# Kernel tuning notes

Measured on AMD Instinct MI355X. Metric: run time of the kernel, lower is better.

The kernel has to match this reference:

```python
import jax, jax.numpy as jnp
import numpy as np

N = 100000   # total nodes in batch
E = 400000   # total directed edges
G = 4096     # number of graphs
D = 300      # emb_dim
H = 600      # GIN MLP hidden = 2*emb_dim
L = 5        # num_layer
BN_EPS = 1e-5
SELF_LOOP_BOND_TYPE = 4  # contextpred convention


def setup_inputs() -> dict:
    key = jax.random.key(0)
    ks = jax.random.split(key, 16)
    s = 0.1
    return {
        "x": jax.random.randint(ks[0], (N, 2), 0, 3),
        "edge_index": jax.random.randint(ks[1], (2, E), 0, N),
        "edge_attr": jax.random.randint(ks[2], (E, 2), 0, 3),
        "batch": jnp.sort(jax.random.randint(ks[3], (N,), 0, G)),
        "atom_emb1": jax.random.normal(ks[4], (120, D), jnp.float32) * s,
        "atom_emb2": jax.random.normal(ks[5], (3, D), jnp.float32) * s,
        "edge_emb1": jax.random.normal(ks[6], (L, 6, D), jnp.float32) * s,
        "edge_emb2": jax.random.normal(ks[7], (L, 3, D), jnp.float32) * s,
        "w1": jax.random.normal(ks[8], (L, D, H), jnp.float32) * (1.0 / np.sqrt(D)),
        "b1": jnp.zeros((L, H), jnp.float32),
        "w2": jax.random.normal(ks[9], (L, H, D), jnp.float32) * (1.0 / np.sqrt(H)),
        "b2": jnp.zeros((L, D), jnp.float32),
        "bn_g": jnp.ones((L, D), jnp.float32),
        "bn_b": jnp.zeros((L, D), jnp.float32),
        "bn_m": jnp.zeros((L, D), jnp.float32),
        "bn_v": jnp.ones((L, D), jnp.float32),
        "head_w1": jax.random.normal(ks[10], (D, 512), jnp.float32) * (1.0 / np.sqrt(D)),
        "head_b1": jnp.zeros((512,), jnp.float32),
        "head_w2": jax.random.normal(ks[11], (512, 2), jnp.float32) * (1.0 / np.sqrt(512)),
        "head_b2": jnp.zeros((2,), jnp.float32),
    }


def _gnn_forward(x, edge_index, edge_attr, batch,
                 atom_emb1, atom_emb2, edge_emb1, edge_emb2,
                 w1, b1, w2, b2, bn_g, bn_b, bn_m, bn_v,
                 head_w1, head_b1, head_w2, head_b2):
    src, dst = edge_index[0], edge_index[1]
    # node input embedding: atom type + chirality
    h = atom_emb1[x[:, 0]] + atom_emb2[x[:, 1]]  # [N, D]
    for l in range(L):
        # edge embeddings for real edges
        eemb = edge_emb1[l][edge_attr[:, 0]] + edge_emb2[l][edge_attr[:, 1]]  # [E, D]
        # self-loop edge embedding (bond type 4, direction 0), same for all nodes
        self_emb = edge_emb1[l][SELF_LOOP_BOND_TYPE] + edge_emb2[l][0]  # [D]
        # GIN 'add' aggregation of messages (x_j + edge_emb), incl. self loops
        agg = jax.ops.segment_sum(h[src] + eemb, dst, num_segments=N)
        agg = agg + h + self_emb  # fused self-loop contribution
        # MLP: Linear(D,2D) -> ReLU -> Linear(2D,D)
        h = jax.nn.relu(agg @ w1[l] + b1[l]) @ w2[l] + b2[l]
        # BatchNorm1d in eval mode (running stats)
        h = (h - bn_m[l]) * jax.lax.rsqrt(bn_v[l] + BN_EPS) * bn_g[l] + bn_b[l]
        if l < L - 1:  # JK='last': ReLU on all but last layer
            h = jax.nn.relu(h)
    # to_dense_batch + sum(axis=1) == segment sum over graphs
    pooled = jax.ops.segment_sum(h, batch, num_segments=G)  # [G, D]
    # task head
    logits = jax.nn.relu(pooled @ head_w1 + head_b1) @ head_w2 + head_b2  # [G, 2]
    return logits


def reference(x, edge_index, edge_attr, batch,
              atom_emb1, atom_emb2, edge_emb1, edge_emb2,
              w1, b1, w2, b2, bn_g, bn_b, bn_m, bn_v,
              head_w1, head_b1, head_w2, head_b2):
    return _gnn_forward(x, edge_index, edge_attr, batch,
                        atom_emb1, atom_emb2, edge_emb1, edge_emb2,
                        w1, b1, w2, b2, bn_g, bn_b, bn_m, bn_v,
                        head_w1, head_b1, head_w2, head_b2)
```

## Files before the change

kernel.cpp:

```cpp
#include <hip/hip_runtime.h>
#include <hip/hip_bf16.h>
#include <stdint.h>

#define N_NODES 100000
#define N_EDGES 400000
#define N_GRAPH 4096
#define DIMD    300
#define NLAYER  5
#define HPAD   304
#define KP1    320
#define W1ROWS 640
#define WID2   320
#define MROWS  64
#define HGR    64

typedef __attribute__((ext_vector_type(8))) short bf16x8_t;
typedef __attribute__((ext_vector_type(4))) float f32x4_t;

__device__ __forceinline__ void gload_lds16(const void* g, void* l) {
  auto gp = (__attribute__((address_space(1))) void*)(uintptr_t)g;
  auto lp = (__attribute__((address_space(3))) void*)(uint32_t)(uintptr_t)l;
  __builtin_amdgcn_global_load_lds(gp, lp, 16, 0, 0);
}
__device__ __forceinline__ short f2bs(float f) {
  __hip_bfloat16 b = __float2bfloat16(f); return *(short*)&b;
}
__device__ __forceinline__ float bs2f(short s) {
  __hip_bfloat16 b; *(short*)&b = s; return __bfloat162float(b);
}
__device__ __forceinline__ void soft_barrier() {
  asm volatile("s_waitcnt lgkmcnt(0)" ::: "memory");
  __builtin_amdgcn_s_barrier();
}

__global__ void k_hist(const int* __restrict__ ei, int* __restrict__ cur) {
  const int e = blockIdx.x * blockDim.x + threadIdx.x;
  if (e < N_EDGES) atomicAdd(&cur[ei[N_EDGES + e]], 1);
}

__global__ void k_scan1(int* __restrict__ cur, int* __restrict__ off, int* __restrict__ bsum) {
  __shared__ int buf[1024];
  const int tid = threadIdx.x;
  const int i = blockIdx.x * 1024 + tid;
  int v = (i < N_NODES) ? cur[i] : 0;
  buf[tid] = v;
  __syncthreads();
  for (int s = 1; s < 1024; s <<= 1) {
    int t = (tid >= s) ? buf[tid - s] : 0;
    __syncthreads();
    buf[tid] += t;
    __syncthreads();
  }
  if (i < N_NODES) { off[i + 1] = buf[tid]; cur[i] = 0; }
  if (tid == 1023) bsum[blockIdx.x] = buf[1023];
}

__global__ void k_scan2(int* __restrict__ bsum, int nb) {
  if (threadIdx.x == 0 && blockIdx.x == 0) {
    int run = 0;
    for (int b = 0; b < nb; ++b) { int v = bsum[b]; bsum[b] = run; run += v; }
  }
}

__global__ void k_scan3(int* __restrict__ off, const int* __restrict__ bsum) {
  const int i = blockIdx.x * blockDim.x + threadIdx.x;
  if (i == 0) off[0] = 0;
  if (i < N_NODES) off[i + 1] += bsum[i >> 10];
}

__global__ void k_fill(const int* __restrict__ ei, const int* __restrict__ ea,
                       const int* __restrict__ off, int* __restrict__ cur,
                       int* __restrict__ csr) {
  const int e = blockIdx.x * blockDim.x + threadIdx.x;
  if (e < N_EDGES) {
    const int d = ei[N_EDGES + e];
    const int pos = atomicAdd(&cur[d], 1);
    const int c = ea[2 * e] * 3 + ea[2 * e + 1];
    csr[off[d] + pos] = (ei[e] << 4) | c;
  }
}

__global__ void k_comb(const float* __restrict__ e1, const float* __restrict__ e2,
                       float* __restrict__ comb) {
  const int idx = blockIdx.x * blockDim.x + threadIdx.x;
  if (idx >= NLAYER * 10 * HPAD) return;
  const int l = idx / (10 * HPAD);
  const int r = (idx / HPAD) % 10;
  const int d = idx % HPAD;
  float v = 0.f;
  if (d < DIMD) {
    int a, b;
    if (r < 9) { a = r / 3; b = r % 3; } else { a = 4; b = 0; }
    v = e1[(l * 6 + a) * DIMD + d] + e2[(l * 3 + b) * DIMD + d];
  }
  comb[idx] = v;
}

__global__ void k_wc1(const float* __restrict__ w, __hip_bfloat16* __restrict__ wb) {
  const int idx = blockIdx.x * blockDim.x + threadIdx.x;
  if (idx >= NLAYER * W1ROWS * KP1) return;
  const int l = idx / (W1ROWS * KP1);
  const int n = (idx / KP1) % W1ROWS;
  const int k = idx % KP1;
  float v = 0.f;
  if (n < 600 && k < DIMD) v = w[((long)l * DIMD + k) * 600 + n];
  wb[idx] = __float2bfloat16(v);
}

__global__ void k_wc2(const float* __restrict__ w, __hip_bfloat16* __restrict__ wb) {
  const int idx = blockIdx.x * blockDim.x + threadIdx.x;
  if (idx >= NLAYER * WID2 * W1ROWS) return;
  const int l = idx / (WID2 * W1ROWS);
  const int n = (idx / W1ROWS) % WID2;
  const int k = idx % W1ROWS;
  float v = 0.f;
  if (n < DIMD && k < 600) v = w[((long)l * 600 + k) * DIMD + n];
  wb[idx] = __float2bfloat16(v);
}

__global__ void k_wch(const float* __restrict__ w, __hip_bfloat16* __restrict__ wb) {
  const int idx = blockIdx.x * blockDim.x + threadIdx.x;
  if (idx >= 512 * KP1) return;
  const int n = idx / KP1;
  const int k = idx % KP1;
  float v = (k < DIMD) ? w[(long)k * 512 + n] : 0.f;
  wb[idx] = __float2bfloat16(v);
}

__global__ void k_nemb(const int* __restrict__ x, const float* __restrict__ ae1,
                       const float* __restrict__ ae2, __hip_bfloat16* __restrict__ h) {
  const int gid = blockIdx.x * blockDim.x + threadIdx.x;
  if (gid >= N_NODES * 38) return;
  const int node = gid / 38;
  const int l = gid % 38;
  bf16x8_t ov;
#pragma unroll
  for (int j = 0; j < 8; ++j) ov[j] = 0;
  {
    const int i0 = x[2 * node], i1 = x[2 * node + 1];
    const float* r1 = ae1 + (long)i0 * DIMD + l * 8;
    const float* r2 = ae2 + (long)i1 * DIMD + l * 8;
#pragma unroll
    for (int j = 0; j < 8; ++j) {
      const int d = l * 8 + j;
      if (d < DIMD) ov[j] = f2bs(r1[j] + r2[j]);
    }
  }
  *(bf16x8_t*)(h + (long)node * HPAD + l * 8) = ov;
}

__global__ __launch_bounds__(256)
void k_agg(const __hip_bfloat16* __restrict__ h, __hip_bfloat16* __restrict__ aggb,
           const int* __restrict__ csr, const int* __restrict__ off,
           const float* __restrict__ comb) {
  const int wv = threadIdx.x >> 6;
  const int lane = threadIdx.x & 63;
  const int node = blockIdx.x * 4 + wv;
  if (node >= N_NODES) return;
  if (lane >= 40) return;
  const bool act = lane < 38;
  float acc[8];
  if (act) {
    const bf16x8_t hv = *(const bf16x8_t*)(h + (long)node * HPAD + lane * 8);
    const float* c9 = comb + 9 * HPAD + lane * 8;
#pragma unroll
    for (int j = 0; j < 8; ++j) acc[j] = bs2f(hv[j]) + c9[j];
  } else {
#pragma unroll
    for (int j = 0; j < 8; ++j) acc[j] = 0.f;
  }
  const int p0 = off[node], p1 = off[node + 1];
  int p = p0;
  for (; p + 1 < p1; p += 2) {
    const int v0 = csr[p], v1 = csr[p + 1];
    if (act) {
      const bf16x8_t h0 = *(const bf16x8_t*)(h + (long)(v0 >> 4) * HPAD + lane * 8);
      const bf16x8_t h1 = *(const bf16x8_t*)(h + (long)(v1 >> 4) * HPAD + lane * 8);
      const float* c0 = comb + (v0 & 15) * HPAD + lane * 8;
      const float* c1 = comb + (v1 & 15) * HPAD + lane * 8;
#pragma unroll
      for (int j = 0; j < 8; ++j) acc[j] += bs2f(h0[j]) + c0[j];
#pragma unroll
      for (int j = 0; j < 8; ++j) acc[j] += bs2f(h1[j]) + c1[j];
    }
  }
  if (p < p1) {
    const int v0 = csr[p];
    if (act) {
      const bf16x8_t h0 = *(const bf16x8_t*)(h + (long)(v0 >> 4) * HPAD + lane * 8);
      const float* c0 = comb + (v0 & 15) * HPAD + lane * 8;
#pragma unroll
      for (int j = 0; j < 8; ++j) acc[j] += bs2f(h0[j]) + c0[j];
    }
  }
  bf16x8_t ov;
#pragma unroll
  for (int j = 0; j < 8; ++j) ov[j] = act ? f2bs(acc[j]) : (short)0;
  *(bf16x8_t*)(aggb + (long)node * KP1 + lane * 8) = ov;
}

__global__ __launch_bounds__(256)
void k_mlp(const __hip_bfloat16* __restrict__ aggb,
           const __hip_bfloat16* __restrict__ w1b,
           const __hip_bfloat16* __restrict__ w2b,
           const float* __restrict__ b1,
           const float* __restrict__ b2,
           const float* __restrict__ bng, const float* __restrict__ bnb,
           const float* __restrict__ bnm, const float* __restrict__ bnv,
           int reluFlag,
           __hip_bfloat16* __restrict__ h) {
  __shared__ __align__(16) char As[MROWS * 640];
  __shared__ __align__(16) char P[2 * MROWS * 256];
  const int tid = threadIdx.x;
  const int lane = tid & 63;
  const int wc = tid >> 6;
  const int fr = lane & 15;
  const int kg = lane >> 4;
  const int row0 = blockIdx.x * MROWS;

#pragma unroll
  for (int it = 0; it < 10; ++it) {
    const int g = it * 256 + tid;
    const int r = g / 40;
    const int gin = g - r * 40;
    int ar = row0 + r;
    if (ar >= N_NODES) ar = N_NODES - 1;
    gload_lds16((const char*)aggb + (size_t)ar * 640 + (size_t)((gin ^ (r & 7)) * 16),
                As + g * 16);
  }

  f32x4_t accB[4][5];
#pragma unroll
  for (int m = 0; m < 4; ++m)
#pragma unroll
    for (int n = 0; n < 5; ++n) accB[m][n] = (f32x4_t){0.f, 0.f, 0.f, 0.f};

  __syncthreads();

  {
    f32x4_t accA[4][2];
#pragma unroll
    for (int m = 0; m < 4; ++m)
#pragma unroll
      for (int n = 0; n < 2; ++n) accA[m][n] = (f32x4_t){0.f, 0.f, 0.f, 0.f};
    const __hip_bfloat16* w1c = w1b + (size_t)(wc * 32) * KP1;
#pragma unroll
    for (int ks = 0; ks < 10; ++ks) {
      const int k2 = ks * 64 + kg * 16;
      bf16x8_t af[4], bfr[2];
#pragma unroll
      for (int m = 0; m < 4; ++m) {
        const int r = m * 16 + fr;
        af[m] = *(const bf16x8_t*)(As + r * 640 + (k2 ^ ((r & 7) << 4)));
      }
#pragma unroll
      for (int n = 0; n < 2; ++n)
        bfr[n] = *(const bf16x8_t*)(w1c + (size_t)(n * 16 + fr) * KP1 + ks * 32 + kg * 8);
#pragma unroll
      for (int m = 0; m < 4; ++m)
#pragma unroll
        for (int n = 0; n < 2; ++n)
          accA[m][n] = __builtin_amdgcn_mfma_f32_16x16x32_bf16(af[m], bfr[n], accA[m][n], 0, 0, 0);
    }
#pragma unroll
    for (int n = 0; n < 2; ++n) {
      const int col = wc * 32 + n * 16 + fr;
      const float bv = (col < 600) ? b1[col] : 0.f;
#pragma unroll
      for (int m = 0; m < 4; ++m)
#pragma unroll
        for (int j = 0; j < 4; ++j) {
          const int prow = m * 16 + kg * 4 + j;
          const int pcol = wc * 32 + n * 16 + fr;
          *(short*)(P + prow * 256 + ((pcol * 2) ^ ((prow & 7) << 4))) =
              f2bs(fmaxf(accA[m][n][j] + bv, 0.f));
        }
    }
  }
  soft_barrier();

#pragma unroll
  for (int c = 0; c < 5; ++c) {
    const char* Pc = P + (c & 1) * (MROWS * 256);
    char* Pn = P + ((c + 1) & 1) * (MROWS * 256);

    bf16x8_t w1f[10];
    if (c < 4) {
      const __hip_bfloat16* w1c = w1b + (size_t)((c + 1) * 128 + wc * 32) * KP1;
#pragma unroll
      for (int ks = 0; ks < 5; ++ks)
#pragma unroll
        for (int n = 0; n < 2; ++n)
          w1f[ks * 2 + n] = *(const bf16x8_t*)(w1c + (size_t)(n * 16 + fr) * KP1 + ks * 32 + kg * 8);
    }

#pragma unroll
    for (int ks = 0; ks < 4; ++ks) {
      bf16x8_t af2[4], bf2[5];
#pragma unroll
      for (int m = 0; m < 4; ++m) {
        const int pr = m * 16 + fr;
        af2[m] = *(const bf16x8_t*)(Pc + pr * 256 + ((ks * 64 + kg * 16) ^ ((pr & 7) << 4)));
      }
      const int k2 = c * 128 + ks * 32 + kg * 8;
#pragma unroll
      for (int n = 0; n < 5; ++n)
        bf2[n] = *(const bf16x8_t*)(w2b + (size_t)(wc * 80 + n * 16 + fr) * W1ROWS + k2);
#pragma unroll
      for (int m = 0; m < 4; ++m)
#pragma unroll
        for (int n = 0; n < 5; ++n)
          accB[m][n] = __builtin_amdgcn_mfma_f32_16x16x32_bf16(af2[m], bf2[n], accB[m][n], 0, 0, 0);
    }

    if (c < 4) {
      f32x4_t accA[4][2];
#pragma unroll
      for (int m = 0; m < 4; ++m)
#pragma unroll
        for (int n = 0; n < 2; ++n) accA[m][n] = (f32x4_t){0.f, 0.f, 0.f, 0.f};
      const __hip_bfloat16* w1c = w1b + (size_t)((c + 1) * 128 + wc * 32) * KP1;
#pragma unroll
      for (int ks = 0; ks < 5; ++ks) {
        const int k2 = ks * 64 + kg * 16;
        bf16x8_t af[4];
#pragma unroll
        for (int m = 0; m < 4; ++m) {
          const int r = m * 16 + fr;
          af[m] = *(const bf16x8_t*)(As + r * 640 + (k2 ^ ((r & 7) << 4)));
        }
#pragma unroll
        for (int m = 0; m < 4; ++m)
#pragma unroll
          for (int n = 0; n < 2; ++n)
            accA[m][n] = __builtin_amdgcn_mfma_f32_16x16x32_bf16(af[m], w1f[ks * 2 + n], accA[m][n], 0, 0, 0);
      }
#pragma unroll
      for (int ks = 5; ks < 10; ++ks) {
        const int k2 = ks * 64 + kg * 16;
        bf16x8_t af[4], bfr[2];
#pragma unroll
        for (int m = 0; m < 4; ++m) {
          const int r = m * 16 + fr;
          af[m] = *(const bf16x8_t*)(As + r * 640 + (k2 ^ ((r & 7) << 4)));
        }
#pragma unroll
        for (int n = 0; n < 2; ++n)
          bfr[n] = *(const bf16x8_t*)(w1c + (size_t)(n * 16 + fr) * KP1 + ks * 32 + kg * 8);
#pragma unroll
        for (int m = 0; m < 4; ++m)
#pragma unroll
          for (int n = 0; n < 2; ++n)
            accA[m][n] = __builtin_amdgcn_mfma_f32_16x16x32_bf16(af[m], bfr[n], accA[m][n], 0, 0, 0);
      }
#pragma unroll
      for (int n = 0; n < 2; ++n) {
        const int col = (c + 1) * 128 + wc * 32 + n * 16 + fr;
        const float bv = (col < 600) ? b1[col] : 0.f;
#pragma unroll
        for (int m = 0; m < 4; ++m)
#pragma unroll
          for (int j = 0; j < 4; ++j) {
            const int prow = m * 16 + kg * 4 + j;
            const int pcol = wc * 32 + n * 16 + fr;
            *(short*)(Pn + prow * 256 + ((pcol * 2) ^ ((prow & 7) << 4))) =
                f2bs(fmaxf(accA[m][n][j] + bv, 0.f));
          }
      }
    }
    soft_barrier();
  }

  float scale[5], shift[5];
#pragma unroll
  for (int n = 0; n < 5; ++n) {
    const int col = wc * 80 + n * 16 + fr;
    if (col < DIMD) {
      const float sc = rsqrtf(bnv[col] + 1e-5f) * bng[col];
      scale[n] = sc;
      shift[n] = (b2[col] - bnm[col]) * sc + bnb[col];
    } else { scale[n] = 0.f; shift[n] = 0.f; }
  }
#pragma unroll
  for (int m = 0; m < 4; ++m) {
#pragma unroll
    for (int n = 0; n < 5; ++n) {
      const int col = wc * 80 + n * 16 + fr;
      if (col >= HPAD) continue;
#pragma unroll
      for (int j = 0; j < 4; ++j) {
        const int node = row0 + m * 16 + kg * 4 + j;
        if (node >= N_NODES) continue;
        float v = 0.f;
        if (col < DIMD) {
          v = accB[m][n][j] * scale[n] + shift[n];
          if (reluFlag) v = fmaxf(v, 0.f);
        }
        h[(size_t)node * HPAD + col] = __float2bfloat16(v);
      }
    }
  }
}

__device__ __forceinline__ int lbound(const int* a, int n, int key) {
  int lo = 0, hi = n;
  while (lo < hi) { int mid = (lo + hi) >> 1; if (a[mid] < key) lo = mid + 1; else hi = mid; }
  return lo;
}

__global__ void k_pool(const __hip_bfloat16* __restrict__ h, const int* __restrict__ batch,
                       __hip_bfloat16* __restrict__ pooled) {
  __shared__ int se[2];
  const int g = blockIdx.x;
  if (threadIdx.x < 2) se[threadIdx.x] = lbound(batch, N_NODES, g + threadIdx.x);
  __syncthreads();
  const int d = threadIdx.x;
  if (d < KP1) {
    float a = 0.f;
    if (d < DIMD)
      for (int i = se[0]; i < se[1]; ++i) a += __bfloat162float(h[(long)i * HPAD + d]);
    pooled[(long)g * KP1 + d] = __float2bfloat16(d < DIMD ? a : 0.f);
  }
}

__global__ __launch_bounds__(256)
void k_head(const __hip_bfloat16* __restrict__ pooled,
            const __hip_bfloat16* __restrict__ hw1b,
            const float* __restrict__ hb1, const float* __restrict__ hw2,
            const float* __restrict__ hb2, float* __restrict__ out) {
  __shared__ __align__(16) char As[HGR * 640];
  __shared__ float sred[4][HGR][2];
  const int tid = threadIdx.x;
  const int lane = tid & 63;
  const int wc = tid >> 6;
  const int fr = lane & 15;
  const int kg = lane >> 4;
  const int g0 = blockIdx.x * HGR;

#pragma unroll
  for (int it = 0; it < 10; ++it) {
    const int g = it * 256 + tid;
    const int r = g / 40;
    const int gin = g - r * 40;
    gload_lds16((const char*)pooled + (size_t)(g0 + r) * 640 + (size_t)((gin ^ (r & 7)) * 16),
                As + g * 16);
  }

  f32x4_t acc[4][8];
#pragma unroll
  for (int m = 0; m < 4; ++m)
#pragma unroll
    for (int n = 0; n < 8; ++n) acc[m][n] = (f32x4_t){0.f, 0.f, 0.f, 0.f};

  __syncthreads();

#pragma unroll
  for (int ks = 0; ks < 10; ++ks) {
    const int k2 = ks * 64 + kg * 16;
    bf16x8_t af[4], bw[8];
#pragma unroll
    for (int m = 0; m < 4; ++m) {
      const int r = m * 16 + fr;
      af[m] = *(const bf16x8_t*)(As + r * 640 + (k2 ^ ((r & 7) << 4)));
    }
#pragma unroll
    for (int n = 0; n < 8; ++n)
      bw[n] = *(const bf16x8_t*)(hw1b + (size_t)(wc * 128 + n * 16 + fr) * KP1 + ks * 32 + kg * 8);
#pragma unroll
    for (int m = 0; m < 4; ++m)
#pragma unroll
      for (int n = 0; n < 8; ++n)
        acc[m][n] = __builtin_amdgcn_mfma_f32_16x16x32_bf16(af[m], bw[n], acc[m][n], 0, 0, 0);
  }

  float p0[4][4], p1[4][4];
#pragma unroll
  for (int m = 0; m < 4; ++m)
#pragma unroll
    for (int j = 0; j < 4; ++j) { p0[m][j] = 0.f; p1[m][j] = 0.f; }
#pragma unroll
  for (int n = 0; n < 8; ++n) {
    const int col = wc * 128 + n * 16 + fr;
    const float bv = hb1[col];
    const float wa = hw2[2 * col], wb = hw2[2 * col + 1];
#pragma unroll
    for (int m = 0; m < 4; ++m)
#pragma unroll
      for (int j = 0; j < 4; ++j) {
        const float z = fmaxf(acc[m][n][j] + bv, 0.f);
        p0[m][j] = fmaf(z, wa, p0[m][j]);
        p1[m][j] = fmaf(z, wb, p1[m][j]);
      }
  }
#pragma unroll
  for (int m = 0; m < 4; ++m)
#pragma unroll
    for (int j = 0; j < 4; ++j) {
#pragma unroll
      for (int s = 1; s < 16; s <<= 1) {
        p0[m][j] += __shfl_xor(p0[m][j], s, 64);
        p1[m][j] += __shfl_xor(p1[m][j], s, 64);
      }
    }
  if (fr == 0) {
#pragma unroll
    for (int m = 0; m < 4; ++m)
#pragma unroll
      for (int j = 0; j < 4; ++j) {
        const int row = m * 16 + kg * 4 + j;
        sred[wc][row][0] = p0[m][j];
        sred[wc][row][1] = p1[m][j];
      }
  }
  __syncthreads();
  if (tid < HGR) {
    const int row = tid;
    float a0 = sred[0][row][0] + sred[1][row][0] + sred[2][row][0] + sred[3][row][0];
    float a1 = sred[0][row][1] + sred[1][row][1] + sred[2][row][1] + sred[3][row][1];
    out[2 * (g0 + row)] = a0 + hb2[0];
    out[2 * (g0 + row) + 1] = a1 + hb2[1];
  }
}

__global__ void k_sentinel(float* out) { out[threadIdx.x] = 1.0e6f; }

extern "C" void kernel_launch(void* const* d_in, const int* in_sizes, int n_in,
                              void* d_out, int out_size, void* d_ws, size_t ws_size,
                              hipStream_t stream) {
  const int*   x     = (const int*)d_in[0];
  const int*   ei    = (const int*)d_in[1];
  const int*   ea    = (const int*)d_in[2];
  const int*   batch = (const int*)d_in[3];
  const float* ae1   = (const float*)d_in[4];
  const float* ae2   = (const float*)d_in[5];
  const float* ee1   = (const float*)d_in[6];
  const float* ee2   = (const float*)d_in[7];
  const float* w1    = (const float*)d_in[8];
  const float* b1    = (const float*)d_in[9];
  const float* w2    = (const float*)d_in[10];
  const float* b2    = (const float*)d_in[11];
  const float* bng   = (const float*)d_in[12];
  const float* bnbp  = (const float*)d_in[13];
  const float* bnm   = (const float*)d_in[14];
  const float* bnv   = (const float*)d_in[15];
  const float* hw1   = (const float*)d_in[16];
  const float* hb1   = (const float*)d_in[17];
  const float* hw2   = (const float*)d_in[18];
  const float* hb2   = (const float*)d_in[19];
  float* out = (float*)d_out;

  char* ws = (char*)d_ws;
  size_t o = 0;
  auto alloc = [&](size_t bytes) { size_t p = o; o += (bytes + 255) & ~(size_t)255; return p; };
  __hip_bfloat16* h      = (__hip_bfloat16*)(ws + alloc((size_t)N_NODES * HPAD * 2));
  __hip_bfloat16* aggb   = (__hip_bfloat16*)(ws + alloc((size_t)N_NODES * KP1 * 2));
  __hip_bfloat16* w1b    = (__hip_bfloat16*)(ws + alloc((size_t)NLAYER * W1ROWS * KP1 * 2));
  __hip_bfloat16* w2b    = (__hip_bfloat16*)(ws + alloc((size_t)NLAYER * WID2 * W1ROWS * 2));
  __hip_bfloat16* hw1b   = (__hip_bfloat16*)(ws + alloc((size_t)512 * KP1 * 2));
  float*          comb   = (float*)         (ws + alloc((size_t)NLAYER * 10 * HPAD * 4));
  int*            offp   = (int*)           (ws + alloc((size_t)(N_NODES + 1) * 4));
  int*            cur    = (int*)           (ws + alloc((size_t)N_NODES * 4));
  int*            csr    = (int*)           (ws + alloc((size_t)N_EDGES * 4));
  __hip_bfloat16* pooled = (__hip_bfloat16*)(ws + alloc((size_t)N_GRAPH * KP1 * 2));
  int*            bsum   = (int*)           (ws + alloc(128 * 4));
  if (o > ws_size) {
    k_sentinel<<<1, 8, 0, stream>>>(out);
    return;
  }

  hipMemsetAsync(cur, 0, (size_t)N_NODES * 4, stream);

  k_hist<<<(N_EDGES + 255) / 256, 256, 0, stream>>>(ei, cur);
  const int nsb = (N_NODES + 1023) / 1024;
  k_scan1<<<nsb, 1024, 0, stream>>>(cur, offp, bsum);
  k_scan2<<<1, 64, 0, stream>>>(bsum, nsb);
  k_scan3<<<(N_NODES + 255) / 256, 256, 0, stream>>>(offp, bsum);
  k_fill<<<(N_EDGES + 255) / 256, 256, 0, stream>>>(ei, ea, offp, cur, csr);

  k_wc1<<<(NLAYER * W1ROWS * KP1 + 255) / 256, 256, 0, stream>>>(w1, w1b);
  k_wc2<<<(NLAYER * WID2 * W1ROWS + 255) / 256, 256, 0, stream>>>(w2, w2b);
  k_wch<<<(512 * KP1 + 255) / 256, 256, 0, stream>>>(hw1, hw1b);
  k_comb<<<(NLAYER * 10 * HPAD + 255) / 256, 256, 0, stream>>>(ee1, ee2, comb);
  k_nemb<<<(N_NODES * 38 + 255) / 256, 256, 0, stream>>>(x, ae1, ae2, h);

  const int mlpBlocks = (N_NODES + MROWS - 1) / MROWS;
  for (int l = 0; l < NLAYER; ++l) {
    k_agg<<<(N_NODES + 3) / 4, 256, 0, stream>>>(h, aggb, csr, offp, comb + l * 10 * HPAD);
    k_mlp<<<mlpBlocks, 256, 0, stream>>>(aggb,
        w1b + (size_t)l * W1ROWS * KP1, w2b + (size_t)l * WID2 * W1ROWS,
        b1 + l * 600, b2 + l * DIMD,
        bng + l * DIMD, bnbp + l * DIMD, bnm + l * DIMD, bnv + l * DIMD,
        (l < NLAYER - 1) ? 1 : 0, h);
  }

  k_pool<<<N_GRAPH, KP1, 0, stream>>>(h, batch, pooled);
  k_head<<<N_GRAPH / HGR, 256, 0, stream>>>(pooled, hw1b, hb1, hw2, hb2, out);
}
```

Baseline: 1.782 ms.

## Replace double-buffered 128-col MLP chunks with simple 64-col loop and two barriers

Restructures the fused MLP kernel's hidden-dimension loop. The old version used double-buffered 128-column chunks of the hidden activation, with W1 fragments prefetched into registers and split GEMM1 stages. The new version uses a plain rolled loop over ten 64-column chunks, a single-buffered P tile that is half the size, and two full __syncthreads per chunk. This cuts LDS use and register pressure (fewer accumulators and no prefetch array), which may raise occupancy. In exchange it gives up the overlap between the two GEMMs and adds more barriers.

```diff
diff --git a/kernel.cpp b/kernel.cpp
--- a/kernel.cpp
+++ b/kernel.cpp
@@ -27,10 +27,6 @@
 }
 __device__ __forceinline__ float bs2f(short s) {
   __hip_bfloat16 b; *(short*)&b = s; return __bfloat162float(b);
-}
-__device__ __forceinline__ void soft_barrier() {
-  asm volatile("s_waitcnt lgkmcnt(0)" ::: "memory");
-  __builtin_amdgcn_s_barrier();
 }
 
 __global__ void k_hist(const int* __restrict__ ei, int* __restrict__ cur) {
@@ -210,7 +206,7 @@
            int reluFlag,
            __hip_bfloat16* __restrict__ h) {
   __shared__ __align__(16) char As[MROWS * 640];
-  __shared__ __align__(16) char P[2 * MROWS * 256];
+  __shared__ __align__(16) char P[MROWS * 128];
   const int tid = threadIdx.x;
   const int lane = tid & 63;
   const int wc = tid >> 6;
@@ -237,72 +233,49 @@
 
   __syncthreads();
 
-  {
-    f32x4_t accA[4][2];
-#pragma unroll
-    for (int m = 0; m < 4; ++m)
-#pragma unroll
-      for (int n = 0; n < 2; ++n) accA[m][n] = (f32x4_t){0.f, 0.f, 0.f, 0.f};
-    const __hip_bfloat16* w1c = w1b + (size_t)(wc * 32) * KP1;
+  for (int hc = 0; hc < 10; ++hc) {
+    f32x4_t accA[4];
+#pragma unroll
+    for (int m = 0; m < 4; ++m) accA[m] = (f32x4_t){0.f, 0.f, 0.f, 0.f};
+    const __hip_bfloat16* w1c = w1b + (size_t)(hc * 64 + wc * 16) * KP1;
 #pragma unroll
     for (int ks = 0; ks < 10; ++ks) {
       const int k2 = ks * 64 + kg * 16;
-      bf16x8_t af[4], bfr[2];
+      bf16x8_t af[4];
 #pragma unroll
       for (int m = 0; m < 4; ++m) {
         const int r = m * 16 + fr;
         af[m] = *(const bf16x8_t*)(As + r * 640 + (k2 ^ ((r & 7) << 4)));
       }
-#pragma unroll
-      for (int n = 0; n < 2; ++n)
-        bfr[n] = *(const bf16x8_t*)(w1c + (size_t)(n * 16 + fr) * KP1 + ks * 32 + kg * 8);
+      const bf16x8_t bfr = *(const bf16x8_t*)(w1c + (size_t)fr * KP1 + ks * 32 + kg * 8);
 #pragma unroll
       for (int m = 0; m < 4; ++m)
-#pragma unroll
-        for (int n = 0; n < 2; ++n)
-          accA[m][n] = __builtin_amdgcn_mfma_f32_16x16x32_bf16(af[m], bfr[n], accA[m][n], 0, 0, 0);
-    }
-#pragma unroll
-    for (int n = 0; n < 2; ++n) {
-      const int col = wc * 32 + n * 16 + fr;
-      const float bv = (col < 600) ? b1[col] : 0.f;
-#pragma unroll
-      for (int m = 0; m < 4; ++m)
-#pragma unroll
-        for (int j = 0; j < 4; ++j) {
-          const int prow = m * 16 + kg * 4 + j;
-          const int pcol = wc * 32 + n * 16 + fr;
-          *(short*)(P + prow * 256 + ((pcol * 2) ^ ((prow & 7) << 4))) =
-              f2bs(fmaxf(accA[m][n][j] + bv, 0.f));
-        }
-    }
-  }
-  soft_barrier();
-
-#pragma unroll
-  for (int c = 0; c < 5; ++c) {
-    const char* Pc = P + (c & 1) * (MROWS * 256);
-    char* Pn = P + ((c + 1) & 1) * (MROWS * 256);
-
-    bf16x8_t w1f[10];
-    if (c < 4) {
-      const __hip_bfloat16* w1c = w1b + (size_t)((c + 1) * 128 + wc * 32) * KP1;
-#pragma unroll
-      for (int ks = 0; ks < 5; ++ks)
-#pragma unroll
-        for (int n = 0; n < 2; ++n)
-          w1f[ks * 2 + n] = *(const bf16x8_t*)(w1c + (size_t)(n * 16 + fr) * KP1 + ks * 32 + kg * 8);
-    }
-
-#pragma unroll
-    for (int ks = 0; ks < 4; ++ks) {
+        accA[m] = __builtin_amdgcn_mfma_f32_16x16x32_bf16(af[m], bfr, accA[m], 0, 0, 0);
+    }
+    const int col = hc * 64 + wc * 16 + fr;
+    const float bv = (col < 600) ? b1[col] : 0.f;
+
+    __syncthreads();
+#pragma unroll
+    for (int m = 0; m < 4; ++m)
+#pragma unroll
+      for (int j = 0; j < 4; ++j) {
+        const int prow = m * 16 + kg * 4 + j;
+        const int pcol = wc * 16 + fr;
+        *(short*)(P + prow * 128 + ((pcol * 2) ^ ((prow & 7) << 4))) =
+            f2bs(fmaxf(accA[m][j] + bv, 0.f));
+      }
+    __syncthreads();
+
+#pragma unroll
+    for (int ks = 0; ks < 2; ++ks) {
       bf16x8_t af2[4], bf2[5];
 #pragma unroll
       for (int m = 0; m < 4; ++m) {
         const int pr = m * 16 + fr;
-        af2[m] = *(const bf16x8_t*)(Pc + pr * 256 + ((ks * 64 + kg * 16) ^ ((pr & 7) << 4)));
-      }
-      const int k2 = c * 128 + ks * 32 + kg * 8;
+        af2[m] = *(const bf16x8_t*)(P + pr * 128 + ((ks * 64 + kg * 16) ^ ((pr & 7) << 4)));
+      }
+      const int k2 = hc * 64 + ks * 32 + kg * 8;
 #pragma unroll
       for (int n = 0; n < 5; ++n)
         bf2[n] = *(const bf16x8_t*)(w2b + (size_t)(wc * 80 + n * 16 + fr) * W1ROWS + k2);
@@ -312,63 +285,6 @@
         for (int n = 0; n < 5; ++n)
           accB[m][n] = __builtin_amdgcn_mfma_f32_16x16x32_bf16(af2[m], bf2[n], accB[m][n], 0, 0, 0);
     }
-
-    if (c < 4) {
-      f32x4_t accA[4][2];
-#pragma unroll
-      for (int m = 0; m < 4; ++m)
-#pragma unroll
-        for (int n = 0; n < 2; ++n) accA[m][n] = (f32x4_t){0.f, 0.f, 0.f, 0.f};
-      const __hip_bfloat16* w1c = w1b + (size_t)((c + 1) * 128 + wc * 32) * KP1;
-#pragma unroll
-      for (int ks = 0; ks < 5; ++ks) {
-        const int k2 = ks * 64 + kg * 16;
-        bf16x8_t af[4];
-#pragma unroll
-        for (int m = 0; m < 4; ++m) {
-          const int r = m * 16 + fr;
-          af[m] = *(const bf16x8_t*)(As + r * 640 + (k2 ^ ((r & 7) << 4)));
-        }
-#pragma unroll
-        for (int m = 0; m < 4; ++m)
-#pragma unroll
-          for (int n = 0; n < 2; ++n)
-            accA[m][n] = __builtin_amdgcn_mfma_f32_16x16x32_bf16(af[m], w1f[ks * 2 + n], accA[m][n], 0, 0, 0);
-      }
-#pragma unroll
-      for (int ks = 5; ks < 10; ++ks) {
-        const int k2 = ks * 64 + kg * 16;
-        bf16x8_t af[4], bfr[2];
-#pragma unroll
-        for (int m = 0; m < 4; ++m) {
-          const int r = m * 16 + fr;
-          af[m] = *(const bf16x8_t*)(As + r * 640 + (k2 ^ ((r & 7) << 4)));
-        }
-#pragma unroll
-        for (int n = 0; n < 2; ++n)
-          bfr[n] = *(const bf16x8_t*)(w1c + (size_t)(n * 16 + fr) * KP1 + ks * 32 + kg * 8);
-#pragma unroll
-        for (int m = 0; m < 4; ++m)
-#pragma unroll
-          for (int n = 0; n < 2; ++n)
-            accA[m][n] = __builtin_amdgcn_mfma_f32_16x16x32_bf16(af[m], bfr[n], accA[m][n], 0, 0, 0);
-      }
-#pragma unroll
-      for (int n = 0; n < 2; ++n) {
-        const int col = (c + 1) * 128 + wc * 32 + n * 16 + fr;
-        const float bv = (col < 600) ? b1[col] : 0.f;
-#pragma unroll
-        for (int m = 0; m < 4; ++m)
-#pragma unroll
-          for (int j = 0; j < 4; ++j) {
-            const int prow = m * 16 + kg * 4 + j;
-            const int pcol = wc * 32 + n * 16 + fr;
-            *(short*)(Pn + prow * 256 + ((pcol * 2) ^ ((prow & 7) << 4))) =
-                f2bs(fmaxf(accA[m][n][j] + bv, 0.f));
-          }
-      }
-    }
-    soft_barrier();
   }
 
   float scale[5], shift[5];
```

After: 1.501 ms. 1.19x faster.
